# Optimization experiments

Hardware: AMD Instinct MI355X
Metric: run time of the kernel (lower is better)

Reference implementation:

```python
import jax, jax.numpy as jnp
import numpy as np

D = 1024   # dim_embedding
H = 16     # n_head
HD = D // H


def setup_inputs() -> dict:
    key = jax.random.key(0)
    ks = jax.random.split(key, 5)
    B, T = 2, 2048
    x = jax.random.normal(ks[0], (B, T, D), dtype=jnp.float32)
    e = jax.random.normal(ks[1], (B, T, D), dtype=jnp.float32)
    s = 0.02
    W_en = jax.random.normal(ks[2], (D, 2 * D), dtype=jnp.float32) * s   # c_attn_en (k,v from encoder)
    W_q = jax.random.normal(ks[3], (D, D), dtype=jnp.float32) * s        # c_attn (q from decoder)
    W_o = jax.random.normal(ks[4], (D, D), dtype=jnp.float32) * s        # c_proj
    return {"x": x, "e": e, "W_en": W_en, "W_q": W_q, "W_o": W_o}


def reference(x, e, W_en, W_q, W_o):
    B, T, C = e.shape
    kv = e @ W_en                       # [B,T,2C]
    k, v = jnp.split(kv, 2, axis=-1)    # [B,T,C] each
    q = x @ W_q                         # [B,T,C]
    # reshape to heads: [B,H,T,hd]
    q = q.reshape(B, T, H, HD).transpose(0, 2, 1, 3)
    k = k.reshape(B, T, H, HD).transpose(0, 2, 1, 3)
    v = v.reshape(B, T, H, HD).transpose(0, 2, 1, 3)
    att = jnp.einsum("bhqd,bhkd->bhqk", q, k) * (1.0 / jnp.sqrt(jnp.float32(HD)))
    att = jax.nn.softmax(att, axis=-1)  # dropout=0 (eval)
    y = jnp.einsum("bhqk,bhkd->bhqd", att, v)
    y = y.transpose(0, 2, 1, 3).reshape(B, T, C)
    return y @ W_o
```

## Files before the change

### kernel.cpp

```cpp
#include <hip/hip_runtime.h>

typedef unsigned short u16;
typedef unsigned int u32;
typedef __bf16 bf16x8 __attribute__((ext_vector_type(8)));
typedef float f32x4 __attribute__((ext_vector_type(4)));
typedef float f32x16 __attribute__((ext_vector_type(16)));

#define D_EMB 1024
#define T_SEQ 2048
#define NH 16
#define HD 64

#define GLB(p) ((const __attribute__((address_space(1))) unsigned int*)(p))
#define LDSP(p) ((__attribute__((address_space(3))) unsigned int*)(p))
#define VMCNT(n) asm volatile("s_waitcnt vmcnt(" #n ")" ::: "memory")
#define LGKM0() asm volatile("s_waitcnt lgkmcnt(0)" ::: "memory")

__device__ __forceinline__ u16 f2bf(float f) {
  union { float f; unsigned u; } c; c.f = f;
  unsigned u = c.u;
  unsigned r = (u + 0x7FFFu + ((u >> 16) & 1u)) >> 16;
  return (u16)r;
}
__device__ __forceinline__ u32 fbits(float f) {
  union { float f; unsigned u; } c; c.f = f; return c.u;
}

__global__ __launch_bounds__(256) void prep_kernel(
    const float* __restrict__ x, const float* __restrict__ e,
    const float* __restrict__ W_q, const float* __restrict__ W_en, const float* __restrict__ W_o,
    u16* __restrict__ xb, u16* __restrict__ eb,
    u16* __restrict__ Wqt, u16* __restrict__ Went, u16* __restrict__ Wot) {
  __shared__ float tile[32][33];
  const int bid = blockIdx.x, tid = threadIdx.x;
  if (bid < 8192) {
    const float* in = (bid < 4096) ? x : e;
    u16* out = (bid < 4096) ? xb : eb;
    int i = (bid & 4095) * 256 + tid;
    float4 v = reinterpret_cast<const float4*>(in)[i];
    ushort4 o;
    o.x = f2bf(v.x); o.y = f2bf(v.y); o.z = f2bf(v.z); o.w = f2bf(v.w);
    reinterpret_cast<ushort4*>(out)[i] = o;
    return;
  }
  const float* in; u16* out; int K, N, bx, by;
  int rem = bid - 8192;
  if (rem < 1024)      { in = W_q;  out = Wqt;  K = 1024; N = 1024; bx = rem & 31; by = rem >> 5; }
  else if (rem < 3072) { int r2 = rem - 1024; in = W_en; out = Went; K = 1024; N = 2048; bx = r2 & 63; by = r2 >> 6; }
  else                 { int r3 = rem - 3072; in = W_o;  out = Wot;  K = 1024; N = 1024; bx = r3 & 31; by = r3 >> 5; }
  int tx = tid & 31, ty = tid >> 5;
  int n0 = bx * 32, k0 = by * 32;
#pragma unroll
  for (int s = 0; s < 4; s++)
    tile[ty + 8 * s][tx] = in[(size_t)(k0 + ty + 8 * s) * N + n0 + tx];
  __syncthreads();
#pragma unroll
  for (int s = 0; s < 4; s++)
    out[(size_t)(n0 + ty + 8 * s) * K + k0 + tx] = f2bf(tile[tx][ty + 8 * s]);
}

__global__ __launch_bounds__(256) void proj_kernel(
    const u16* __restrict__ xb, const u16* __restrict__ eb,
    const u16* __restrict__ Wqt, const u16* __restrict__ Went,
    u16* __restrict__ qw, u16* __restrict__ kw, u16* __restrict__ vTw) {
  __shared__ u16 Al[3][128 * 32], Bl[3][128 * 32];
  const int tid = threadIdx.x;
  const int bid0 = blockIdx.y * 24 + blockIdx.x;
  const int wgid = (bid0 & 7) * 96 + (bid0 >> 3);
  const int nb = wgid % 24, mb = wgid / 24;
  const int wave = tid >> 6, lane = tid & 63;
  const int ln15 = lane & 15, quad = lane >> 4;
  const int wm = wave & 1, wn = wave >> 1;

  const u16* A = (nb < 8) ? xb : eb;
  const u16* Wt = (nb < 8) ? (Wqt + (size_t)nb * 128 * D_EMB)
                           : (Went + ((size_t)nb * 128 - D_EMB) * D_EMB);

  const int srow = lane >> 2, sch = lane & 3;
  const int gch = sch ^ ((srow >> 1) & 3);
  const u16* gA = A + (size_t)(mb * 128 + wave * 32 + srow) * D_EMB + gch * 8;
  const u16* gB = Wt + (size_t)(wave * 32 + srow) * D_EMB + gch * 8;

  auto stage = [&](int kb, u16* AL, u16* BL) {
    char* lA = (char*)AL + wave * 2048;
    char* lB = (char*)BL + wave * 2048;
#pragma unroll
    for (int it = 0; it < 2; it++) {
      __builtin_amdgcn_global_load_lds(GLB(gA + (size_t)it * 16 * D_EMB + kb), LDSP(lA + it * 1024), 16, 0, 0);
      __builtin_amdgcn_global_load_lds(GLB(gB + (size_t)it * 16 * D_EMB + kb), LDSP(lB + it * 1024), 16, 0, 0);
    }
  };

  f32x4 acc[4][4] = {};
  bf16x8 af[4], bfr[4];

  auto ldfrag = [&](const u16* AL, const u16* BL) {
#pragma unroll
    for (int mt = 0; mt < 4; mt++) {
      int r = wm * 64 + mt * 16 + ln15;
      af[mt] = *reinterpret_cast<const bf16x8*>(&AL[r * 32 + ((quad ^ ((r >> 1) & 3)) * 8)]);
    }
#pragma unroll
    for (int nt = 0; nt < 4; nt++) {
      int r = wn * 64 + nt * 16 + ln15;
      bfr[nt] = *reinterpret_cast<const bf16x8*>(&BL[r * 32 + ((quad ^ ((r >> 1) & 3)) * 8)]);
    }
  };
  auto domfma = [&]() {
    __builtin_amdgcn_s_setprio(1);
#pragma unroll
    for (int mt = 0; mt < 4; mt++)
#pragma unroll
      for (int nt = 0; nt < 4; nt++)
        acc[mt][nt] = __builtin_amdgcn_mfma_f32_16x16x32_bf16(af[mt], bfr[nt], acc[mt][nt], 0, 0, 0);
    __builtin_amdgcn_s_setprio(0);
  };

  stage(0,  Al[0], Bl[0]);
  stage(32, Al[1], Bl[1]);
  stage(64, Al[2], Bl[2]);
  u16 *cA = Al[0], *cB = Bl[0], *nA = Al[1], *nB = Bl[1], *mA = Al[2], *mB = Bl[2];

  for (int kb = 0; kb < 928; kb += 32) {
    VMCNT(8);
    __builtin_amdgcn_s_barrier();
    ldfrag(cA, cB);
    LGKM0();
    __builtin_amdgcn_s_barrier();
    stage(kb + 96, cA, cB);
    domfma();
    u16* t;
    t = cA; cA = nA; nA = mA; mA = t;
    t = cB; cB = nB; nB = mB; mB = t;
  }
  VMCNT(8); __builtin_amdgcn_s_barrier(); ldfrag(cA, cB); domfma();
  VMCNT(4); __builtin_amdgcn_s_barrier(); ldfrag(nA, nB); domfma();
  VMCNT(0); __builtin_amdgcn_s_barrier(); ldfrag(mA, mB); domfma();

  const float QSCL = 0.125f * 1.44269504f;
#pragma unroll
  for (int mt = 0; mt < 4; mt++) {
#pragma unroll
    for (int nt = 0; nt < 4; nt++) {
#pragma unroll
      for (int i = 0; i < 4; i++) {
        int rr = mb * 128 + wm * 64 + mt * 16 + quad * 4 + i;
        int c  = nb * 128 + wn * 64 + nt * 16 + ln15;
        float v = acc[mt][nt][i];
        int b = rr >> 11, t = rr & 2047;
        if (c < D_EMB) {
          int h = c >> 6, d = c & 63;
          qw[(((size_t)(b * NH + h)) * T_SEQ + t) * HD + d] = f2bf(v * QSCL);
        } else if (c < 2 * D_EMB) {
          int cc = c - D_EMB; int h = cc >> 6, d = cc & 63;
          kw[(((size_t)(b * NH + h)) * T_SEQ + t) * HD + d] = f2bf(v);
        } else {
          int cc = c - 2 * D_EMB; int h = cc >> 6, d = cc & 63;
          vTw[(((size_t)(b * NH + h)) * HD + d) * T_SEQ + t] = f2bf(v);
        }
      }
    }
  }
}

__global__ __launch_bounds__(256) void attn_kernel(
    const u16* __restrict__ q, const u16* __restrict__ k,
    const u16* __restrict__ vT, u16* __restrict__ y) {
  __shared__ u16 Kl[3][64][64], Vl[3][64][64];

  const int bid0 = blockIdx.x;
  const int wgid = (bid0 & 7) * 64 + (bid0 >> 3);
  const int bh = wgid >> 4;
  const int qt = wgid & 15;
  const int tid = threadIdx.x;
  const int wave = tid >> 6, lane = tid & 63;
  const int q32 = lane & 31, hi = lane >> 5;
  const int b = bh >> 4, h = bh & 15;

  const int pq = (q32 & 19) | ((q32 & 8) >> 1) | ((q32 & 4) << 1);
  const int pq7 = pq & 7;

  const int qrow = qt * 128 + wave * 32 + q32;
  const u16* qbase = q + ((size_t)bh * T_SEQ + qrow) * HD;
  bf16x8 qf[4];
#pragma unroll
  for (int s = 0; s < 4; s++)
    qf[s] = *reinterpret_cast<const bf16x8*>(qbase + s * 16 + hi * 8);

  f32x16 o2[2] = {};
  float lp = 0.f;

  const int srow = (lane >> 3) & 7;
  const int gch  = (lane & 7) ^ srow;
  const u16* kg0 = k  + ((size_t)bh * T_SEQ + wave * 16 + srow) * HD + gch * 8;
  const u16* vg0 = vT + ((size_t)bh * HD + wave * 16 + srow) * T_SEQ + gch * 8;

  auto issue_dma = [&](int t, u16 (*KL)[64], u16 (*VL)[64]) {
    char* klb = (char*)KL + wave * 2048;
    char* vlb = (char*)VL + wave * 2048;
    const u16* kp = kg0 + (size_t)t * 64 * HD;
    const u16* vp = vg0 + t * 64;
    __builtin_amdgcn_global_load_lds(GLB(kp),             LDSP(klb),        16, 0, 0);
    __builtin_amdgcn_global_load_lds(GLB(kp + 8 * HD),    LDSP(klb + 1024), 16, 0, 0);
    __builtin_amdgcn_global_load_lds(GLB(vp),             LDSP(vlb),        16, 0, 0);
    __builtin_amdgcn_global_load_lds(GLB(vp + 8 * T_SEQ), LDSP(vlb + 1024), 16, 0, 0);
  };

  auto body = [&](const u16 (*KL)[64], const u16 (*VL)[64]) {
    f32x16 s2[2] = {};
    __builtin_amdgcn_s_setprio(1);
#pragma unroll
    for (int s = 0; s < 4; s++)
#pragma unroll
      for (int kt2 = 0; kt2 < 2; kt2++) {
        int r = kt2 * 32 + pq;
        bf16x8 kf = *reinterpret_cast<const bf16x8*>(&KL[r][(((s * 2 + hi) ^ pq7) * 8)]);
        s2[kt2] = __builtin_amdgcn_mfma_f32_32x32x16_bf16(kf, qf[s], s2[kt2], 0, 0, 0);
      }

#pragma unroll
    for (int s = 0; s < 4; s++) {
      const int kt2 = s >> 1;
      const int g0 = (2 * s) & 3;
      float e0 = __builtin_amdgcn_exp2f(s2[kt2][4 * g0 + 0]);
      float e1 = __builtin_amdgcn_exp2f(s2[kt2][4 * g0 + 1]);
      float e2 = __builtin_amdgcn_exp2f(s2[kt2][4 * g0 + 2]);
      float e3 = __builtin_amdgcn_exp2f(s2[kt2][4 * g0 + 3]);
      float e4 = __builtin_amdgcn_exp2f(s2[kt2][4 * g0 + 4]);
      float e5 = __builtin_amdgcn_exp2f(s2[kt2][4 * g0 + 5]);
      float e6 = __builtin_amdgcn_exp2f(s2[kt2][4 * g0 + 6]);
      float e7 = __builtin_amdgcn_exp2f(s2[kt2][4 * g0 + 7]);
      lp += ((e0 + e1) + (e2 + e3)) + ((e4 + e5) + (e6 + e7));
      u32 w0 = __builtin_amdgcn_perm(fbits(e1), fbits(e0), 0x07060302u);
      u32 w1 = __builtin_amdgcn_perm(fbits(e3), fbits(e2), 0x07060302u);
      u32 w2 = __builtin_amdgcn_perm(fbits(e5), fbits(e4), 0x07060302u);
      u32 w3 = __builtin_amdgcn_perm(fbits(e7), fbits(e6), 0x07060302u);
      union { u32 w[4]; bf16x8 v; } pu;
      pu.w[0] = w0; pu.w[1] = w1; pu.w[2] = w2; pu.w[3] = w3;
      bf16x8 pf = pu.v;
#pragma unroll
      for (int dt = 0; dt < 2; dt++) {
        int r = dt * 32 + q32;
        bf16x8 vf = *reinterpret_cast<const bf16x8*>(&VL[r][(((s * 2 + hi) ^ (r & 7)) * 8)]);
        o2[dt] = __builtin_amdgcn_mfma_f32_32x32x16_bf16(vf, pf, o2[dt], 0, 0, 0);
      }
    }
    __builtin_amdgcn_s_setprio(0);
  };

  issue_dma(0, Kl[0], Vl[0]);
  issue_dma(1, Kl[1], Vl[1]);
  issue_dma(2, Kl[2], Vl[2]);
  u16 (*cK)[64] = Kl[0]; u16 (*cV)[64] = Vl[0];
  u16 (*nK)[64] = Kl[1]; u16 (*nV)[64] = Vl[1];
  u16 (*mK)[64] = Kl[2]; u16 (*mV)[64] = Vl[2];

  for (int t = 0; t < 29; t++) {
    VMCNT(8);
    __builtin_amdgcn_s_barrier();
    body(cK, cV);
    LGKM0();
    __builtin_amdgcn_s_barrier();
    issue_dma(t + 3, cK, cV);
    u16 (*tp)[64];
    tp = cK; cK = nK; nK = mK; mK = tp;
    tp = cV; cV = nV; nV = mV; mV = tp;
  }
  VMCNT(8); __builtin_amdgcn_s_barrier(); body(cK, cV);
  VMCNT(4); __builtin_amdgcn_s_barrier(); body(nK, nV);
  VMCNT(0); __builtin_amdgcn_s_barrier(); body(mK, mV);

  lp += __shfl_xor(lp, 32, 64);
  const float inv = 1.0f / lp;

  const size_t ybase = ((size_t)b * T_SEQ + qrow) * D_EMB + h * 64;
#pragma unroll
  for (int dt = 0; dt < 2; dt++)
#pragma unroll
    for (int g = 0; g < 4; g++) {
      u16 b0 = f2bf(o2[dt][4 * g + 0] * inv), b1 = f2bf(o2[dt][4 * g + 1] * inv);
      u16 b2 = f2bf(o2[dt][4 * g + 2] * inv), b3 = f2bf(o2[dt][4 * g + 3] * inv);
      u32 dw0 = (u32)b0 | ((u32)b1 << 16);
      u32 dw1 = (u32)b2 | ((u32)b3 << 16);
      *reinterpret_cast<uint2*>(&y[ybase + dt * 32 + 8 * g + 4 * hi]) = make_uint2(dw0, dw1);
    }
}

__global__ __launch_bounds__(256) void oproj_kernel(
    const u16* __restrict__ yw, const u16* __restrict__ Wot, float* __restrict__ out) {
  __shared__ u16 Al[3][64 * 32], Bl[3][128 * 32];
  const int tid = threadIdx.x;
  const int bid0 = blockIdx.y * 8 + blockIdx.x;
  const int wgid = (bid0 & 7) * 64 + (bid0 >> 3);
  const int nb = wgid & 7, mb = wgid >> 3;
  const int wave = tid >> 6, lane = tid & 63;
  const int ln15 = lane & 15, quad = lane >> 4;
  const int wm = wave & 1, wn = wave >> 1;

  const int srow = lane >> 2, sch = lane & 3;
  const int gch = sch ^ ((srow >> 1) & 3);
  const u16* gA = yw  + (size_t)(mb * 64 + wave * 16 + srow) * D_EMB + gch * 8;
  const u16* gB = Wot + (size_t)(nb * 128 + wave * 32 + srow) * D_EMB + gch * 8;

  auto stage = [&](int kb, u16* AL, u16* BL) {
    char* lA = (char*)AL + wave * 1024;
    char* lB = (char*)BL + wave * 2048;
    __builtin_amdgcn_global_load_lds(GLB(gA + kb), LDSP(lA), 16, 0, 0);
#pragma unroll
    for (int it = 0; it < 2; it++)
      __builtin_amdgcn_global_load_lds(GLB(gB + (size_t)it * 16 * D_EMB + kb), LDSP(lB + it * 1024), 16, 0, 0);
  };

  f32x4 acc[2][4] = {};
  bf16x8 af[2], bfr[4];

  auto ldfrag = [&](const u16* AL, const u16* BL) {
#pragma unroll
    for (int mt = 0; mt < 2; mt++) {
      int r = wm * 32 + mt * 16 + ln15;
      af[mt] = *reinterpret_cast<const bf16x8*>(&AL[r * 32 + ((quad ^ ((r >> 1) & 3)) * 8)]);
    }
#pragma unroll
    for (int nt = 0; nt < 4; nt++) {
      int r = wn * 64 + nt * 16 + ln15;
      bfr[nt] = *reinterpret_cast<const bf16x8*>(&BL[r * 32 + ((quad ^ ((r >> 1) & 3)) * 8)]);
    }
  };
  auto domfma = [&]() {
    __builtin_amdgcn_s_setprio(1);
#pragma unroll
    for (int mt = 0; mt < 2; mt++)
#pragma unroll
      for (int nt = 0; nt < 4; nt++)
        acc[mt][nt] = __builtin_amdgcn_mfma_f32_16x16x32_bf16(af[mt], bfr[nt], acc[mt][nt], 0, 0, 0);
    __builtin_amdgcn_s_setprio(0);
  };

  stage(0,  Al[0], Bl[0]);
  stage(32, Al[1], Bl[1]);
  stage(64, Al[2], Bl[2]);
  u16 *cA = Al[0], *cB = Bl[0], *nA = Al[1], *nB = Bl[1], *mA = Al[2], *mB = Bl[2];

  for (int kb = 0; kb < 928; kb += 32) {
    VMCNT(6);
    __builtin_amdgcn_s_barrier();
    ldfrag(cA, cB);
    LGKM0();
    __builtin_amdgcn_s_barrier();
    stage(kb + 96, cA, cB);
    domfma();
    u16* t;
    t = cA; cA = nA; nA = mA; mA = t;
    t = cB; cB = nB; nB = mB; mB = t;
  }
  VMCNT(6); __builtin_amdgcn_s_barrier(); ldfrag(cA, cB); domfma();
  VMCNT(3); __builtin_amdgcn_s_barrier(); ldfrag(nA, nB); domfma();
  VMCNT(0); __builtin_amdgcn_s_barrier(); ldfrag(mA, mB); domfma();

#pragma unroll
  for (int mt = 0; mt < 2; mt++)
#pragma unroll
    for (int nt = 0; nt < 4; nt++)
#pragma unroll
      for (int i = 0; i < 4; i++) {
        int rr = mb * 64 + wm * 32 + mt * 16 + quad * 4 + i;
        int c  = nb * 128 + wn * 64 + nt * 16 + ln15;
        out[(size_t)rr * D_EMB + c] = acc[mt][nt][i];
      }
}

extern "C" void kernel_launch(void* const* d_in, const int* in_sizes, int n_in,
                              void* d_out, int out_size, void* d_ws, size_t ws_size,
                              hipStream_t stream) {
  const float* x    = (const float*)d_in[0];
  const float* e    = (const float*)d_in[1];
  const float* W_en = (const float*)d_in[2];
  const float* W_q  = (const float*)d_in[3];
  const float* W_o  = (const float*)d_in[4];
  float* out = (float*)d_out;

  char* w = (char*)d_ws;
  u16* xb   = (u16*)(w);
  u16* eb   = (u16*)(w + (8u  << 20));
  u16* Wqt  = (u16*)(w + (16u << 20));
  u16* Went = (u16*)(w + (18u << 20));
  u16* Wot  = (u16*)(w + (22u << 20));
  u16* qw   = (u16*)(w + (24u << 20));
  u16* kw   = (u16*)(w + (32u << 20));
  u16* vT   = (u16*)(w + (40u << 20));
  u16* yw   = (u16*)(w + (48u << 20));

  prep_kernel<<<12288, 256, 0, stream>>>(x, e, W_q, W_en, W_o, xb, eb, Wqt, Went, Wot);
  proj_kernel<<<dim3(24, 32), 256, 0, stream>>>(xb, eb, Wqt, Went, qw, kw, vT);
  attn_kernel<<<512, 256, 0, stream>>>(qw, kw, vT, yw);
  oproj_kernel<<<dim3(8, 64), 256, 0, stream>>>(yw, Wot, out);
}
```

Before: 189.5 us.

## Simplify projection GEMM to double-buffered loop and widen weight-transpose tiles

Result: slower. 196.0 us (+3.4%).

```diff
diff --git a/kernel.cpp b/kernel.cpp
--- a/kernel.cpp
+++ b/kernel.cpp
@@ -31,7 +31,7 @@
     const float* __restrict__ W_q, const float* __restrict__ W_en, const float* __restrict__ W_o,
     u16* __restrict__ xb, u16* __restrict__ eb,
     u16* __restrict__ Wqt, u16* __restrict__ Went, u16* __restrict__ Wot) {
-  __shared__ float tile[32][33];
+  __shared__ float tile[64][65];
   const int bid = blockIdx.x, tid = threadIdx.x;
   if (bid < 8192) {
     const float* in = (bid < 4096) ? x : e;
@@ -45,29 +45,40 @@
   }
   const float* in; u16* out; int K, N, bx, by;
   int rem = bid - 8192;
-  if (rem < 1024)      { in = W_q;  out = Wqt;  K = 1024; N = 1024; bx = rem & 31; by = rem >> 5; }
-  else if (rem < 3072) { int r2 = rem - 1024; in = W_en; out = Went; K = 1024; N = 2048; bx = r2 & 63; by = r2 >> 6; }
-  else                 { int r3 = rem - 3072; in = W_o;  out = Wot;  K = 1024; N = 1024; bx = r3 & 31; by = r3 >> 5; }
-  int tx = tid & 31, ty = tid >> 5;
-  int n0 = bx * 32, k0 = by * 32;
-#pragma unroll
-  for (int s = 0; s < 4; s++)
-    tile[ty + 8 * s][tx] = in[(size_t)(k0 + ty + 8 * s) * N + n0 + tx];
+  if (rem < 256)      { in = W_q;  out = Wqt;  K = 1024; N = 1024; bx = rem & 15; by = rem >> 4; }
+  else if (rem < 768) { int r2 = rem - 256; in = W_en; out = Went; K = 1024; N = 2048; bx = r2 & 31; by = r2 >> 5; }
+  else                { int r3 = rem - 768; in = W_o;  out = Wot;  K = 1024; N = 1024; bx = r3 & 15; by = r3 >> 4; }
+  const int t15 = tid & 15, t16 = tid >> 4;
+  const int n0 = bx * 64, k0 = by * 64;
+#pragma unroll
+  for (int s = 0; s < 4; s++) {
+    float4 v = reinterpret_cast<const float4*>(&in[(size_t)(k0 + t16 + 16 * s) * N + n0])[t15];
+    tile[t16 + 16 * s][4 * t15 + 0] = v.x;
+    tile[t16 + 16 * s][4 * t15 + 1] = v.y;
+    tile[t16 + 16 * s][4 * t15 + 2] = v.z;
+    tile[t16 + 16 * s][4 * t15 + 3] = v.w;
+  }
   __syncthreads();
 #pragma unroll
-  for (int s = 0; s < 4; s++)
-    out[(size_t)(n0 + ty + 8 * s) * K + k0 + tx] = f2bf(tile[tx][ty + 8 * s]);
+  for (int s = 0; s < 4; s++) {
+    int n = t16 + 16 * s;
+    ushort4 o;
+    o.x = f2bf(tile[4 * t15 + 0][n]);
+    o.y = f2bf(tile[4 * t15 + 1][n]);
+    o.z = f2bf(tile[4 * t15 + 2][n]);
+    o.w = f2bf(tile[4 * t15 + 3][n]);
+    *reinterpret_cast<ushort4*>(&out[(size_t)(n0 + n) * K + k0 + 4 * t15]) = o;
+  }
 }
 
 __global__ __launch_bounds__(256) void proj_kernel(
     const u16* __restrict__ xb, const u16* __restrict__ eb,
     const u16* __restrict__ Wqt, const u16* __restrict__ Went,
     u16* __restrict__ qw, u16* __restrict__ kw, u16* __restrict__ vTw) {
-  __shared__ u16 Al[3][128 * 32], Bl[3][128 * 32];
+  __shared__ u16 Al0[128 * 32], Bl0[128 * 32];
+  __shared__ u16 Al1[128 * 32], Bl1[128 * 32];
   const int tid = threadIdx.x;
-  const int bid0 = blockIdx.y * 24 + blockIdx.x;
-  const int wgid = (bid0 & 7) * 96 + (bid0 >> 3);
-  const int nb = wgid % 24, mb = wgid / 24;
+  const int nb = blockIdx.x, mb = blockIdx.y;
   const int wave = tid >> 6, lane = tid & 63;
   const int ln15 = lane & 15, quad = lane >> 4;
   const int wm = wave & 1, wn = wave >> 1;
@@ -92,9 +103,9 @@
   };
 
   f32x4 acc[4][4] = {};
-  bf16x8 af[4], bfr[4];
-
-  auto ldfrag = [&](const u16* AL, const u16* BL) {
+
+  auto compute = [&](const u16* AL, const u16* BL) {
+    bf16x8 af[4], bfr[4];
 #pragma unroll
     for (int mt = 0; mt < 4; mt++) {
       int r = wm * 64 + mt * 16 + ln15;
@@ -105,37 +116,22 @@
       int r = wn * 64 + nt * 16 + ln15;
       bfr[nt] = *reinterpret_cast<const bf16x8*>(&BL[r * 32 + ((quad ^ ((r >> 1) & 3)) * 8)]);
     }
-  };
-  auto domfma = [&]() {
-    __builtin_amdgcn_s_setprio(1);
 #pragma unroll
     for (int mt = 0; mt < 4; mt++)
 #pragma unroll
       for (int nt = 0; nt < 4; nt++)
         acc[mt][nt] = __builtin_amdgcn_mfma_f32_16x16x32_bf16(af[mt], bfr[nt], acc[mt][nt], 0, 0, 0);
-    __builtin_amdgcn_s_setprio(0);
-  };
-
-  stage(0,  Al[0], Bl[0]);
-  stage(32, Al[1], Bl[1]);
-  stage(64, Al[2], Bl[2]);
-  u16 *cA = Al[0], *cB = Bl[0], *nA = Al[1], *nB = Bl[1], *mA = Al[2], *mB = Bl[2];
-
-  for (int kb = 0; kb < 928; kb += 32) {
-    VMCNT(8);
-    __builtin_amdgcn_s_barrier();
-    ldfrag(cA, cB);
-    LGKM0();
-    __builtin_amdgcn_s_barrier();
-    stage(kb + 96, cA, cB);
-    domfma();
-    u16* t;
-    t = cA; cA = nA; nA = mA; mA = t;
-    t = cB; cB = nB; nB = mB; mB = t;
-  }
-  VMCNT(8); __builtin_amdgcn_s_barrier(); ldfrag(cA, cB); domfma();
-  VMCNT(4); __builtin_amdgcn_s_barrier(); ldfrag(nA, nB); domfma();
-  VMCNT(0); __builtin_amdgcn_s_barrier(); ldfrag(mA, mB); domfma();
+  };
+
+  stage(0, Al0, Bl0);
+  for (int kb = 0; kb < D_EMB; kb += 64) {
+    __syncthreads();
+    stage(kb + 32, Al1, Bl1);
+    compute(Al0, Bl0);
+    __syncthreads();
+    if (kb + 64 < D_EMB) stage(kb + 64, Al0, Bl0);
+    compute(Al1, Bl1);
+  }
 
   const float QSCL = 0.125f * 1.44269504f;
 #pragma unroll
@@ -390,7 +386,7 @@
   u16* vT   = (u16*)(w + (40u << 20));
   u16* yw   = (u16*)(w + (48u << 20));
 
-  prep_kernel<<<12288, 256, 0, stream>>>(x, e, W_q, W_en, W_o, xb, eb, Wqt, Went, Wot);
+  prep_kernel<<<9216, 256, 0, stream>>>(x, e, W_q, W_en, W_o, xb, eb, Wqt, Went, Wot);
   proj_kernel<<<dim3(24, 32), 256, 0, stream>>>(xb, eb, Wqt, Went, qw, kw, vT);
   attn_kernel<<<512, 256, 0, stream>>>(qw, kw, vT, yw);
   oproj_kernel<<<dim3(8, 64), 256, 0, stream>>>(yw, Wot, out);
```
